# Optimization experiments

Measured on AMD Instinct MI355X. Metric: run time of the kernel, lower is better.

Reference implementation:

```python
import jax, jax.numpy as jnp
import numpy as np

DIM_H = 128
HEADS = 8
HEAD_DIM = DIM_H // HEADS
N_NODES = 40000
N_EDGES = 640000
BN_EPS = 1e-5


def setup_inputs() -> dict:
    key = jax.random.key(0)
    ks = jax.random.split(key, 16)
    s = 0.05
    x = jax.random.normal(ks[0], (N_NODES, DIM_H), dtype=jnp.float32)
    edge_index = jax.random.randint(ks[1], (2, N_EDGES), 0, N_NODES, dtype=jnp.int64)
    p = lambda k, shp: jax.random.normal(k, shp, dtype=jnp.float32) * s
    return {
        "x": x,
        "edge_index": edge_index,
        "Wk": p(ks[2], (DIM_H, DIM_H)), "bk": p(ks[3], (DIM_H,)),
        "Wv": p(ks[4], (DIM_H, DIM_H)), "bv": p(ks[5], (DIM_H,)),
        "Wo": p(ks[6], (DIM_H, DIM_H)), "bo": p(ks[7], (DIM_H,)),
        "bn1_g": jnp.ones((DIM_H,), jnp.float32), "bn1_b": jnp.zeros((DIM_H,), jnp.float32),
        "W1": p(ks[8], (2 * DIM_H, DIM_H)), "b1": p(ks[9], (2 * DIM_H,)),
        "W2": p(ks[10], (DIM_H, 2 * DIM_H)), "b2": p(ks[11], (DIM_H,)),
        "bn2_g": jnp.ones((DIM_H,), jnp.float32), "bn2_b": jnp.zeros((DIM_H,), jnp.float32),
    }


def _batchnorm(h, gamma, beta):
    # BatchNorm1d in training mode: per-feature batch mean / biased var over nodes
    mu = jnp.mean(h, axis=0)
    var = jnp.mean((h - mu) ** 2, axis=0)
    return (h - mu) * jax.lax.rsqrt(var + BN_EPS) * gamma + beta


def _sparse_attn(x, edge_index, Wk, bk, Wv, bv, Wo, bo):
    N = x.shape[0]
    src, dst = edge_index[0], edge_index[1]
    K = (x @ Wk.T + bk).reshape(N, HEADS, HEAD_DIM)
    V = (x @ Wv.T + bv).reshape(N, HEADS, HEAD_DIM)
    Q = x.reshape(N, HEADS, HEAD_DIM)  # query is raw h (no projection)
    # per-edge scores [E, H]
    scores = jnp.sum(K[src] * Q[dst], axis=-1) / np.sqrt(HEAD_DIM).astype(np.float32)
    # segment softmax over destination nodes (pyg_softmax)
    m = jax.ops.segment_max(scores, dst, num_segments=N)
    e = jnp.exp(scores - m[dst])
    denom = jax.ops.segment_sum(e, dst, num_segments=N)
    attn = e / (denom[dst] + 1e-16)  # [E, H]
    messages = V[src] * attn[:, :, None]  # [E, H, D]
    out = jax.ops.segment_sum(messages, dst, num_segments=N)  # [N, H, D]
    return out.reshape(N, DIM_H) @ Wo.T + bo


def reference(x, edge_index, Wk, bk, Wv, bv, Wo, bo, bn1_g, bn1_b,
              W1, b1, W2, b2, bn2_g, bn2_b):
    h_attn = _sparse_attn(x, edge_index, Wk, bk, Wv, bv, Wo, bo)
    h = _batchnorm(x + h_attn, bn1_g, bn1_b)
    ff = jax.nn.relu(h @ W1.T + b1) @ W2.T + b2
    h = _batchnorm(h + ff, bn2_g, bn2_b)
    return h
```

## Files before the change

### kernel.cpp

```cpp
#include <hip/hip_runtime.h>

#define DIM 128

typedef __attribute__((ext_vector_type(4))) _Float16 half4;
typedef __attribute__((ext_vector_type(8))) _Float16 half8;
typedef __attribute__((ext_vector_type(4))) float f32x4;

#define HP 136
#define UP 264

__global__ __launch_bounds__(256) void conv_wall(const float* __restrict__ Wk,
    const float* __restrict__ Wv, const float* __restrict__ Wo,
    const float* __restrict__ W1, const float* __restrict__ W2,
    _Float16* __restrict__ Wkh, _Float16* __restrict__ Wvh,
    _Float16* __restrict__ Woh, _Float16* __restrict__ W1h,
    _Float16* __restrict__ W2h, int* __restrict__ cnt, float* __restrict__ stats,
    int N) {
  int i = blockIdx.x * 256 + threadIdx.x;
  if (i < 16384) Wkh[i] = (_Float16)Wk[i];
  else if (i < 32768) Wvh[i - 16384] = (_Float16)Wv[i - 16384];
  else if (i < 49152) Woh[i - 32768] = (_Float16)Wo[i - 32768];
  else if (i < 81920) W1h[i - 49152] = (_Float16)W1[i - 49152];
  else W2h[i - 81920] = (_Float16)W2[i - 81920];
  if (i < N) cnt[i] = 0;
  if (i < 512) stats[i] = 0.f;
}

__global__ __launch_bounds__(256) void kv_mfma(const float* __restrict__ x,
    const _Float16* __restrict__ Wkh, const float* __restrict__ bk,
    const _Float16* __restrict__ Wvh, const float* __restrict__ bv,
    _Float16* __restrict__ KV, int N) {
  __shared__ _Float16 xs[64 * HP];
  int tid = threadIdx.x;
  int base = blockIdx.x * 64;
  int lane = tid & 63, w = tid >> 6;
  int l15 = lane & 15, quad = lane >> 4;

  for (int i = tid; i < 64 * 32; i += 256) {
    int m = i >> 5, c4 = i & 31;
    float4 tv = ((const float4*)x)[(size_t)(base + m) * 32 + c4];
    half4 hv;
    hv.x = (_Float16)tv.x; hv.y = (_Float16)tv.y;
    hv.z = (_Float16)tv.z; hv.w = (_Float16)tv.w;
    *(half4*)&xs[m * HP + c4 * 4] = hv;
  }
  __syncthreads();

  half8 afr[4][4];
#pragma unroll
  for (int mt = 0; mt < 4; mt++)
#pragma unroll
    for (int ks = 0; ks < 4; ks++)
      afr[mt][ks] = *(const half8*)&xs[(mt * 16 + l15) * HP + ks * 32 + quad * 8];

  const _Float16* W = (w < 2) ? Wkh : Wvh;
  const float* bias = (w < 2) ? bk : bv;
  int voff = (w < 2) ? 0 : 4;
  int c0 = (w & 1) * 64;

#pragma unroll
  for (int nt = 0; nt < 4; nt++) {
    int f = c0 + nt * 16 + l15;
    half8 bfr[4];
#pragma unroll
    for (int ks = 0; ks < 4; ks++)
      bfr[ks] = *(const half8*)&W[(size_t)f * 128 + ks * 32 + quad * 8];
    f32x4 acc[4];
#pragma unroll
    for (int mt = 0; mt < 4; mt++) acc[mt] = (f32x4){0.f, 0.f, 0.f, 0.f};
#pragma unroll
    for (int ks = 0; ks < 4; ks++)
#pragma unroll
      for (int mt = 0; mt < 4; mt++)
        acc[mt] = __builtin_amdgcn_mfma_f32_16x16x32_f16(afr[mt][ks], bfr[ks],
                                                          acc[mt], 0, 0, 0);
    float bb = bias[f];
    int fo = (f >> 2) * 8 + (f & 3) + voff;
#pragma unroll
    for (int mt = 0; mt < 4; mt++)
#pragma unroll
      for (int r = 0; r < 4; r++)
        KV[(size_t)(base + mt * 16 + quad * 4 + r) * 256 + fo] =
            (_Float16)(acc[mt][r] + bb);
  }
}

__global__ __launch_bounds__(256) void hist_rank(const int* __restrict__ ei,
    int* __restrict__ cnt, int* __restrict__ rank, int E) {
  int e = blockIdx.x * 256 + threadIdx.x;
  if (e < E) rank[e] = atomicAdd(&cnt[ei[E + e]], 1);
}

__global__ __launch_bounds__(256) void scanA(const int* __restrict__ cnt,
    int* __restrict__ rs, int* __restrict__ bsum, int N) {
  __shared__ int s[256];
  int t = threadIdx.x;
  int i = blockIdx.x * 256 + t;
  int v = (i < N) ? cnt[i] : 0;
  s[t] = v;
  __syncthreads();
  for (int off = 1; off < 256; off <<= 1) {
    int add = (t >= off) ? s[t - off] : 0;
    __syncthreads();
    s[t] += add;
    __syncthreads();
  }
  if (i < N) rs[i] = s[t] - v;
  if (t == 255) bsum[blockIdx.x] = s[t];
}

__global__ __launch_bounds__(256) void scanB(int* __restrict__ bsum, int nb) {
  __shared__ int s[256];
  int t = threadIdx.x;
  int v = (t < nb) ? bsum[t] : 0;
  s[t] = v;
  __syncthreads();
  for (int off = 1; off < 256; off <<= 1) {
    int add = (t >= off) ? s[t - off] : 0;
    __syncthreads();
    s[t] += add;
    __syncthreads();
  }
  if (t < nb) bsum[t] = s[t] - v;
}

__global__ __launch_bounds__(256) void scanC(int* __restrict__ rs,
    const int* __restrict__ bsum, int N, int E) {
  int i = blockIdx.x * 256 + threadIdx.x;
  if (i < N) rs[i] += bsum[blockIdx.x];
  if (i == 0) rs[N] = E;
}

__global__ __launch_bounds__(256) void scatter2(const int* __restrict__ ei,
    const int* __restrict__ rs, const int* __restrict__ rank,
    int* __restrict__ esrc, int E) {
  int e = blockIdx.x * 256 + threadIdx.x;
  if (e < E) esrc[rs[ei[E + e]] + rank[e]] = ei[e];
}

__global__ __launch_bounds__(256) void attn_agg(const _Float16* __restrict__ KV,
    const float* __restrict__ x, const int* __restrict__ rs,
    const int* __restrict__ esrc, _Float16* __restrict__ attn16, int N) {
  int wave = threadIdx.x >> 6, lane = threadIdx.x & 63;
  int n = blockIdx.x * 4 + wave;
  if (n >= N) return;
  int l = lane & 31, s = lane >> 5;
  float4 q = *(const float4*)&x[(size_t)n * DIM + 4 * l];
  int beg = rs[n], end = rs[n + 1];
  float a0 = 0.f, a1 = 0.f, a2 = 0.f, a3 = 0.f, dloc = 0.f;
  for (int e = beg + s; e < end; e += 8) {
    bool hh[4];
    int ss[4];
#pragma unroll
    for (int u = 0; u < 4; u++) hh[u] = (e + 2 * u) < end;
    ss[0] = esrc[e];
#pragma unroll
    for (int u = 1; u < 4; u++) ss[u] = hh[u] ? esrc[e + 2 * u] : ss[0];
    half8 kv[4];
#pragma unroll
    for (int u = 0; u < 4; u++)
      kv[u] = *(const half8*)&KV[(size_t)ss[u] * 256 + 8 * l];
    float p[4];
#pragma unroll
    for (int u = 0; u < 4; u++)
      p[u] = (float)kv[u][0] * q.x + (float)kv[u][1] * q.y +
             (float)kv[u][2] * q.z + (float)kv[u][3] * q.w;
#pragma unroll
    for (int u = 0; u < 4; u++) p[u] += __shfl_xor(p[u], 1);
#pragma unroll
    for (int u = 0; u < 4; u++) p[u] += __shfl_xor(p[u], 2);
    float ev[4];
#pragma unroll
    for (int u = 0; u < 4; u++) ev[u] = hh[u] ? __expf(p[u] * 0.25f) : 0.f;
#pragma unroll
    for (int u = 0; u < 4; u++) {
      dloc += ev[u];
      a0 += ev[u] * (float)kv[u][4];
      a1 += ev[u] * (float)kv[u][5];
      a2 += ev[u] * (float)kv[u][6];
      a3 += ev[u] * (float)kv[u][7];
    }
  }
  dloc += __shfl_xor(dloc, 32);
  a0 += __shfl_xor(a0, 32);
  a1 += __shfl_xor(a1, 32);
  a2 += __shfl_xor(a2, 32);
  a3 += __shfl_xor(a3, 32);
  if (s == 0) {
    float inv = 1.0f / (dloc + 1e-16f);
    half4 o;
    o.x = (_Float16)(a0 * inv);
    o.y = (_Float16)(a1 * inv);
    o.z = (_Float16)(a2 * inv);
    o.w = (_Float16)(a3 * inv);
    *(half4*)&attn16[(size_t)n * DIM + 4 * l] = o;
  }
}

__global__ __launch_bounds__(256) void o_proj_mfma(const _Float16* __restrict__ attn16,
    const float* __restrict__ x, const _Float16* __restrict__ Woh,
    const float* __restrict__ bo, float* __restrict__ t,
    float* __restrict__ stats, int N) {
  __shared__ _Float16 as16[64 * HP];
  int tid = threadIdx.x;
  int base = blockIdx.x * 64;
  int lane = tid & 63, w = tid >> 6;
  int l15 = lane & 15, quad = lane >> 4;

  for (int i = tid; i < 64 * 16; i += 256) {
    int m = i >> 4, c8 = i & 15;
    *(half8*)&as16[m * HP + c8 * 8] =
        ((const half8*)attn16)[(size_t)(base + m) * 16 + c8];
  }
  __syncthreads();

  half8 afr[4][4];
#pragma unroll
  for (int mt = 0; mt < 4; mt++)
#pragma unroll
    for (int ks = 0; ks < 4; ks++)
      afr[mt][ks] = *(const half8*)&as16[(mt * 16 + l15) * HP + ks * 32 + quad * 8];

  int c0 = w * 32;
  f32x4 acc[4][2];
#pragma unroll
  for (int mt = 0; mt < 4; mt++)
#pragma unroll
    for (int nt = 0; nt < 2; nt++) acc[mt][nt] = (f32x4){0.f, 0.f, 0.f, 0.f};
#pragma unroll
  for (int ks = 0; ks < 4; ks++) {
    half8 b[2];
#pragma unroll
    for (int nt = 0; nt < 2; nt++)
      b[nt] = *(const half8*)&Woh[(size_t)(c0 + nt * 16 + l15) * 128 + ks * 32 +
                                  quad * 8];
#pragma unroll
    for (int mt = 0; mt < 4; mt++)
#pragma unroll
      for (int nt = 0; nt < 2; nt++)
        acc[mt][nt] =
            __builtin_amdgcn_mfma_f32_16x16x32_f16(afr[mt][ks], b[nt], acc[mt][nt], 0, 0, 0);
  }

#pragma unroll
  for (int nt = 0; nt < 2; nt++) {
    int f = c0 + nt * 16 + l15;
    float bb = bo[f];
    float s = 0.f, q = 0.f;
#pragma unroll
    for (int mt = 0; mt < 4; mt++) {
#pragma unroll
      for (int r = 0; r < 4; r++) {
        int row = mt * 16 + quad * 4 + r;
        float tv = acc[mt][nt][r] + bb + x[(size_t)(base + row) * DIM + f];
        t[(size_t)(base + row) * DIM + f] = tv;
        s += tv;
        q += tv * tv;
      }
    }
    s += __shfl_xor(s, 16);
    s += __shfl_xor(s, 32);
    q += __shfl_xor(q, 16);
    q += __shfl_xor(q, 32);
    if (quad == 0) {
      atomicAdd(&stats[f], s);
      atomicAdd(&stats[128 + f], q);
    }
  }
}

__global__ __launch_bounds__(256) void ffn_mfma(const float* __restrict__ t,
    const float* __restrict__ stats1, const float* __restrict__ g1,
    const float* __restrict__ bb1, const _Float16* __restrict__ W1h,
    const float* __restrict__ b1, const _Float16* __restrict__ W2h,
    const float* __restrict__ b2, float* __restrict__ z,
    float* __restrict__ stats2, float invN, int N) {
  __shared__ _Float16 hs[64 * HP];
  __shared__ _Float16 us[64 * UP];
  __shared__ float cf[256];
  int tid = threadIdx.x;
  int base = blockIdx.x * 64;
  int lane = tid & 63, w = tid >> 6;
  int l15 = lane & 15, quad = lane >> 4;

  if (tid < 128) {
    float mu = stats1[tid] * invN;
    float var = stats1[128 + tid] * invN - mu * mu;
    float a = rsqrtf(var + 1e-5f) * g1[tid];
    cf[tid] = a;
    cf[128 + tid] = bb1[tid] - mu * a;
  }
  __syncthreads();

  for (int i = tid; i < 64 * 32; i += 256) {
    int m = i >> 5, c4 = i & 31;
    float4 tv = ((const float4*)t)[(size_t)(base + m) * 32 + c4];
    float4 ca = ((const float4*)cf)[c4];
    float4 cc = ((const float4*)cf)[32 + c4];
    half4 hv;
    hv.x = (_Float16)(tv.x * ca.x + cc.x);
    hv.y = (_Float16)(tv.y * ca.y + cc.y);
    hv.z = (_Float16)(tv.z * ca.z + cc.z);
    hv.w = (_Float16)(tv.w * ca.w + cc.w);
    *(half4*)&hs[m * HP + c4 * 4] = hv;
  }
  __syncthreads();

  int n0 = w * 64;
  half8 afr[4][4];
#pragma unroll
  for (int mt = 0; mt < 4; mt++)
#pragma unroll
    for (int ks = 0; ks < 4; ks++)
      afr[mt][ks] = *(const half8*)&hs[(mt * 16 + l15) * HP + ks * 32 + quad * 8];

#pragma unroll
  for (int nt = 0; nt < 4; nt++) {
    int n = n0 + nt * 16 + l15;
    half8 bfr[4];
#pragma unroll
    for (int ks = 0; ks < 4; ks++)
      bfr[ks] = *(const half8*)&W1h[(size_t)n * 128 + ks * 32 + quad * 8];
    f32x4 acc[4];
#pragma unroll
    for (int mt = 0; mt < 4; mt++) acc[mt] = (f32x4){0.f, 0.f, 0.f, 0.f};
#pragma unroll
    for (int ks = 0; ks < 4; ks++)
#pragma unroll
      for (int mt = 0; mt < 4; mt++)
        acc[mt] = __builtin_amdgcn_mfma_f32_16x16x32_f16(afr[mt][ks], bfr[ks],
                                                          acc[mt], 0, 0, 0);
    float bias = b1[n];
#pragma unroll
    for (int mt = 0; mt < 4; mt++)
#pragma unroll
      for (int r = 0; r < 4; r++)
        us[(mt * 16 + quad * 4 + r) * UP + n] =
            (_Float16)fmaxf(acc[mt][r] + bias, 0.f);
  }
  __syncthreads();

  int n2 = w * 32;
  f32x4 acc2[4][2];
#pragma unroll
  for (int mt = 0; mt < 4; mt++)
#pragma unroll
    for (int nt = 0; nt < 2; nt++) acc2[mt][nt] = (f32x4){0.f, 0.f, 0.f, 0.f};
  for (int ks = 0; ks < 8; ks++) {
    half8 a[4], b[2];
#pragma unroll
    for (int mt = 0; mt < 4; mt++)
      a[mt] = *(const half8*)&us[(mt * 16 + l15) * UP + ks * 32 + quad * 8];
#pragma unroll
    for (int nt = 0; nt < 2; nt++)
      b[nt] = *(const half8*)&W2h[(size_t)(n2 + nt * 16 + l15) * 256 + ks * 32 +
                                  quad * 8];
#pragma unroll
    for (int mt = 0; mt < 4; mt++)
#pragma unroll
      for (int nt = 0; nt < 2; nt++)
        acc2[mt][nt] =
            __builtin_amdgcn_mfma_f32_16x16x32_f16(a[mt], b[nt], acc2[mt][nt], 0, 0, 0);
  }

#pragma unroll
  for (int nt = 0; nt < 2; nt++) {
    int f = n2 + nt * 16 + l15;
    float bz = b2[f];
    float s = 0.f, q = 0.f;
#pragma unroll
    for (int mt = 0; mt < 4; mt++) {
#pragma unroll
      for (int r = 0; r < 4; r++) {
        int row = mt * 16 + quad * 4 + r;
        float hv = (float)hs[row * HP + f];
        float zv = hv + acc2[mt][nt][r] + bz;
        z[(size_t)(base + row) * DIM + f] = zv;
        s += zv;
        q += zv * zv;
      }
    }
    s += __shfl_xor(s, 16);
    s += __shfl_xor(s, 32);
    q += __shfl_xor(q, 16);
    q += __shfl_xor(q, 32);
    if (quad == 0) {
      atomicAdd(&stats2[f], s);
      atomicAdd(&stats2[128 + f], q);
    }
  }
}

__global__ __launch_bounds__(256) void final_apply(const float* __restrict__ z,
    const float* __restrict__ stats2, const float* __restrict__ g2,
    const float* __restrict__ bb2, float* __restrict__ out, float invN,
    int total4) {
  __shared__ float cf[256];
  int tid = threadIdx.x;
  if (tid < 128) {
    float mu = stats2[tid] * invN;
    float var = stats2[128 + tid] * invN - mu * mu;
    float a = rsqrtf(var + 1e-5f) * g2[tid];
    cf[tid] = a;
    cf[128 + tid] = bb2[tid] - mu * a;
  }
  __syncthreads();
  int i = blockIdx.x * 256 + tid;
  if (i >= total4) return;
  int f = (i * 4) & 127;
  float4 zv = ((const float4*)z)[i];
  float4 o;
  o.x = zv.x * cf[f] + cf[128 + f];
  o.y = zv.y * cf[f + 1] + cf[128 + f + 1];
  o.z = zv.z * cf[f + 2] + cf[128 + f + 2];
  o.w = zv.w * cf[f + 3] + cf[128 + f + 3];
  ((float4*)out)[i] = o;
}

extern "C" void kernel_launch(void* const* d_in, const int* in_sizes, int n_in,
                              void* d_out, int out_size, void* d_ws, size_t ws_size,
                              hipStream_t stream) {
  const float* x = (const float*)d_in[0];
  const int* ei = (const int*)d_in[1];
  const float* Wk = (const float*)d_in[2];
  const float* bk = (const float*)d_in[3];
  const float* Wv = (const float*)d_in[4];
  const float* bv = (const float*)d_in[5];
  const float* Wo = (const float*)d_in[6];
  const float* bo = (const float*)d_in[7];
  const float* bn1_g = (const float*)d_in[8];
  const float* bn1_b = (const float*)d_in[9];
  const float* W1 = (const float*)d_in[10];
  const float* b1 = (const float*)d_in[11];
  const float* W2 = (const float*)d_in[12];
  const float* b2 = (const float*)d_in[13];
  const float* bn2_g = (const float*)d_in[14];
  const float* bn2_b = (const float*)d_in[15];
  float* out = (float*)d_out;

  int N = in_sizes[0] / DIM;
  int E = in_sizes[1] / 2;

  _Float16* KV = (_Float16*)d_ws;
  _Float16* attn16 = KV + (size_t)N * 256;
  float* zbuf = (float*)(attn16 + (size_t)N * DIM);
  float* tbuf = (float*)d_ws;
  _Float16* W1h = (_Float16*)(zbuf + (size_t)N * DIM);
  _Float16* W2h = W1h + 32768;
  _Float16* Wkh = W2h + 32768;
  _Float16* Wvh = Wkh + 16384;
  _Float16* Woh = Wvh + 16384;
  float* stats = (float*)(Woh + 16384);
  int* cnt = (int*)(stats + 512);
  int* rs = cnt + N;
  int* rank = rs + N + 1;
  int* esrc = rank + E;
  int* bsum = esrc + E;

  int nblk = (N + 255) / 256;
  float invN = 1.0f / N;

  conv_wall<<<448, 256, 0, stream>>>(Wk, Wv, Wo, W1, W2, Wkh, Wvh, Woh, W1h, W2h,
                                     cnt, stats, N);
  kv_mfma<<<N / 64, 256, 0, stream>>>(x, Wkh, bk, Wvh, bv, KV, N);
  hist_rank<<<(E + 255) / 256, 256, 0, stream>>>(ei, cnt, rank, E);
  scanA<<<nblk, 256, 0, stream>>>(cnt, rs, bsum, N);
  scanB<<<1, 256, 0, stream>>>(bsum, nblk);
  scanC<<<nblk, 256, 0, stream>>>(rs, bsum, N, E);
  scatter2<<<(E + 255) / 256, 256, 0, stream>>>(ei, rs, rank, esrc, E);
  attn_agg<<<(N + 3) / 4, 256, 0, stream>>>(KV, x, rs, esrc, attn16, N);
  o_proj_mfma<<<N / 64, 256, 0, stream>>>(attn16, x, Woh, bo, tbuf, stats, N);
  ffn_mfma<<<N / 64, 256, 0, stream>>>(tbuf, stats, bn1_g, bn1_b, W1h, b1, W2h, b2,
                                       zbuf, stats + 256, invN, N);
  final_apply<<<((N * DIM / 4) + 255) / 256, 256, 0, stream>>>(
      zbuf, stats + 256, bn2_g, bn2_b, out, invN, N * DIM / 4);
}
```

Baseline: 260.4 us.

## Fuse CSR build into one cooperative kernel; use fp16 dot2 in attention

The five CSR-construction kernels (histogram/rank, three scan stages, scatter) are merged into a single cooperative kernel that uses grid-wide syncs between phases. The zeroing of counts and stats moves into it as well. This removes several launch gaps at the cost of grid.sync barriers and a fixed 640-block grid. Separately, attn_agg now computes the score dot products with fdot2 on fp16 pairs and accumulates the value-weighted sums in packed half2 rather than fp32. That cuts ALU work but lowers accumulation precision, so high-degree nodes risk larger error or overflow.

```diff
diff --git a/kernel.cpp b/kernel.cpp
--- a/kernel.cpp
+++ b/kernel.cpp
@@ -1,7 +1,11 @@
 #include <hip/hip_runtime.h>
+#include <hip/hip_cooperative_groups.h>
+
+namespace cg = cooperative_groups;
 
 #define DIM 128
 
+typedef __attribute__((ext_vector_type(2))) _Float16 half2_t;
 typedef __attribute__((ext_vector_type(4))) _Float16 half4;
 typedef __attribute__((ext_vector_type(8))) _Float16 half8;
 typedef __attribute__((ext_vector_type(4))) float f32x4;
@@ -14,16 +18,71 @@
     const float* __restrict__ W1, const float* __restrict__ W2,
     _Float16* __restrict__ Wkh, _Float16* __restrict__ Wvh,
     _Float16* __restrict__ Woh, _Float16* __restrict__ W1h,
-    _Float16* __restrict__ W2h, int* __restrict__ cnt, float* __restrict__ stats,
-    int N) {
+    _Float16* __restrict__ W2h) {
   int i = blockIdx.x * 256 + threadIdx.x;
   if (i < 16384) Wkh[i] = (_Float16)Wk[i];
   else if (i < 32768) Wvh[i - 16384] = (_Float16)Wv[i - 16384];
   else if (i < 49152) Woh[i - 32768] = (_Float16)Wo[i - 32768];
   else if (i < 81920) W1h[i - 49152] = (_Float16)W1[i - 49152];
   else W2h[i - 81920] = (_Float16)W2[i - 81920];
-  if (i < N) cnt[i] = 0;
-  if (i < 512) stats[i] = 0.f;
+}
+
+__global__ __launch_bounds__(256) void csr_coop(const int* __restrict__ ei,
+    int* __restrict__ cnt, int* __restrict__ rank, int* __restrict__ rs,
+    int* __restrict__ bsum, int* __restrict__ esrc, float* __restrict__ stats,
+    int N, int E) {
+  cg::grid_group grid = cg::this_grid();
+  __shared__ int sm[256];
+  int t = threadIdx.x;
+  int tid = blockIdx.x * 256 + t;
+  int nth = gridDim.x * 256;
+  int nchunk = (N + 255) / 256;
+
+  for (int i = tid; i < N; i += nth) cnt[i] = 0;
+  if (tid < 512) stats[tid] = 0.f;
+  grid.sync();
+
+  for (int e = tid; e < E; e += nth) rank[e] = atomicAdd(&cnt[ei[E + e]], 1);
+  grid.sync();
+
+  if (blockIdx.x < (unsigned)nchunk) {
+    int i = blockIdx.x * 256 + t;
+    int v = (i < N) ? cnt[i] : 0;
+    sm[t] = v;
+    __syncthreads();
+    for (int off = 1; off < 256; off <<= 1) {
+      int add = (t >= off) ? sm[t - off] : 0;
+      __syncthreads();
+      sm[t] += add;
+      __syncthreads();
+    }
+    if (i < N) rs[i] = sm[t] - v;
+    if (t == 255) bsum[blockIdx.x] = sm[t];
+  }
+  grid.sync();
+
+  if (blockIdx.x == 0) {
+    int v = (t < nchunk) ? bsum[t] : 0;
+    sm[t] = v;
+    __syncthreads();
+    for (int off = 1; off < 256; off <<= 1) {
+      int add = (t >= off) ? sm[t - off] : 0;
+      __syncthreads();
+      sm[t] += add;
+      __syncthreads();
+    }
+    if (t < nchunk) bsum[t] = sm[t] - v;
+  }
+  grid.sync();
+
+  if (blockIdx.x < (unsigned)nchunk) {
+    int i = blockIdx.x * 256 + t;
+    if (i < N) rs[i] += bsum[blockIdx.x];
+  }
+  if (tid == 0) rs[N] = E;
+  grid.sync();
+
+  for (int e = tid; e < E; e += nth) esrc[rs[ei[E + e]] + rank[e]] = ei[e];
 }
 
 __global__ __launch_bounds__(256) void kv_mfma(const float* __restrict__ x,
@@ -85,59 +144,6 @@
   }
 }
 
-__global__ __launch_bounds__(256) void hist_rank(const int* __restrict__ ei,
-    int* __restrict__ cnt, int* __restrict__ rank, int E) {
-  int e = blockIdx.x * 256 + threadIdx.x;
-  if (e < E) rank[e] = atomicAdd(&cnt[ei[E + e]], 1);
-}
-
-__global__ __launch_bounds__(256) void scanA(const int* __restrict__ cnt,
-    int* __restrict__ rs, int* __restrict__ bsum, int N) {
-  __shared__ int s[256];
-  int t = threadIdx.x;
-  int i = blockIdx.x * 256 + t;
-  int v = (i < N) ? cnt[i] : 0;
-  s[t] = v;
-  __syncthreads();
-  for (int off = 1; off < 256; off <<= 1) {
-    int add = (t >= off) ? s[t - off] : 0;
-    __syncthreads();
-    s[t] += add;
-    __syncthreads();
-  }
-  if (i < N) rs[i] = s[t] - v;
-  if (t == 255) bsum[blockIdx.x] = s[t];
-}
-
-__global__ __launch_bounds__(256) void scanB(int* __restrict__ bsum, int nb) {
-  __shared__ int s[256];
-  int t = threadIdx.x;
-  int v = (t < nb) ? bsum[t] : 0;
-  s[t] = v;
-  __syncthreads();
-  for (int off = 1; off < 256; off <<= 1) {
-    int add = (t >= off) ? s[t - off] : 0;
-    __syncthreads();
-    s[t] += add;
-    __syncthreads();
-  }
-  if (t < nb) bsum[t] = s[t] - v;
-}
-
-__global__ __launch_bounds__(256) void scanC(int* __restrict__ rs,
-    const int* __restrict__ bsum, int N, int E) {
-  int i = blockIdx.x * 256 + threadIdx.x;
-  if (i < N) rs[i] += bsum[blockIdx.x];
-  if (i == 0) rs[N] = E;
-}
-
-__global__ __launch_bounds__(256) void scatter2(const int* __restrict__ ei,
-    const int* __restrict__ rs, const int* __restrict__ rank,
-    int* __restrict__ esrc, int E) {
-  int e = blockIdx.x * 256 + threadIdx.x;
-  if (e < E) esrc[rs[ei[E + e]] + rank[e]] = ei[e];
-}
-
 __global__ __launch_bounds__(256) void attn_agg(const _Float16* __restrict__ KV,
     const float* __restrict__ x, const int* __restrict__ rs,
     const int* __restrict__ esrc, _Float16* __restrict__ attn16, int N) {
@@ -146,8 +152,12 @@
   if (n >= N) return;
   int l = lane & 31, s = lane >> 5;
   float4 q = *(const float4*)&x[(size_t)n * DIM + 4 * l];
+  half2_t q01 = {(_Float16)q.x, (_Float16)q.y};
+  half2_t q23 = {(_Float16)q.z, (_Float16)q.w};
   int beg = rs[n], end = rs[n + 1];
-  float a0 = 0.f, a1 = 0.f, a2 = 0.f, a3 = 0.f, dloc = 0.f;
+  half2_t a01 = {(_Float16)0.f, (_Float16)0.f};
+  half2_t a23 = a01;
+  float dloc = 0.f;
   for (int e = beg + s; e < end; e += 8) {
     bool hh[4];
     int ss[4];
@@ -162,25 +172,30 @@
       kv[u] = *(const half8*)&KV[(size_t)ss[u] * 256 + 8 * l];
     float p[4];
 #pragma unroll
-    for (int u = 0; u < 4; u++)
-      p[u] = (float)kv[u][0] * q.x + (float)kv[u][1] * q.y +
-             (float)kv[u][2] * q.z + (float)kv[u][3] * q.w;
+    for (int u = 0; u < 4; u++) {
+      half2_t k01 = {kv[u][0], kv[u][1]};
+      half2_t k23 = {kv[u][2], kv[u][3]};
+      p[u] = __builtin_amdgcn_fdot2(k01, q01,
+              __builtin_amdgcn_fdot2(k23, q23, 0.f, false), false);
+    }
 #pragma unroll
     for (int u = 0; u < 4; u++) p[u] += __shfl_xor(p[u], 1);
 #pragma unroll
     for (int u = 0; u < 4; u++) p[u] += __shfl_xor(p[u], 2);
-    float ev[4];
-#pragma unroll
-    for (int u = 0; u < 4; u++) ev[u] = hh[u] ? __expf(p[u] * 0.25f) : 0.f;
 #pragma unroll
     for (int u = 0; u < 4; u++) {
-      dloc += ev[u];
-      a0 += ev[u] * (float)kv[u][4];
-      a1 += ev[u] * (float)kv[u][5];
-      a2 += ev[u] * (float)kv[u][6];
-      a3 += ev[u] * (float)kv[u][7];
-    }
-  }
+      float ev = hh[u] ? __expf(p[u] * 0.25f) : 0.f;
+      dloc += ev;
+      _Float16 eh = (_Float16)ev;
+      half2_t e2 = {eh, eh};
+      half2_t v01 = {kv[u][4], kv[u][5]};
+      half2_t v23 = {kv[u][6], kv[u][7]};
+      a01 += e2 * v01;
+      a23 += e2 * v23;
+    }
+  }
+  float a0 = (float)a01[0], a1 = (float)a01[1];
+  float a2 = (float)a23[0], a3 = (float)a23[1];
   dloc += __shfl_xor(dloc, 32);
   a0 += __shfl_xor(a0, 32);
   a1 += __shfl_xor(a1, 32);
@@ -457,17 +472,17 @@
   int* esrc = rank + E;
   int* bsum = esrc + E;
 
-  int nblk = (N + 255) / 256;
   float invN = 1.0f / N;
 
-  conv_wall<<<448, 256, 0, stream>>>(Wk, Wv, Wo, W1, W2, Wkh, Wvh, Woh, W1h, W2h,
-                                     cnt, stats, N);
+  conv_wall<<<448, 256, 0, stream>>>(Wk, Wv, Wo, W1, W2, Wkh, Wvh, Woh, W1h, W2h);
   kv_mfma<<<N / 64, 256, 0, stream>>>(x, Wkh, bk, Wvh, bv, KV, N);
-  hist_rank<<<(E + 255) / 256, 256, 0, stream>>>(ei, cnt, rank, E);
-  scanA<<<nblk, 256, 0, stream>>>(cnt, rs, bsum, N);
-  scanB<<<1, 256, 0, stream>>>(bsum, nblk);
-  scanC<<<nblk, 256, 0, stream>>>(rs, bsum, N, E);
-  scatter2<<<(E + 255) / 256, 256, 0, stream>>>(ei, rs, rank, esrc, E);
+  {
+    void* args[] = {(void*)&ei, (void*)&cnt, (void*)&rank, (void*)&rs,
+                    (void*)&bsum, (void*)&esrc, (void*)&stats, (void*)&N,
+                    (void*)&E};
+    hipLaunchCooperativeKernel(reinterpret_cast<void*>(csr_coop), dim3(640),
+                               dim3(256), args, 0, stream);
+  }
   attn_agg<<<(N + 3) / 4, 256, 0, stream>>>(KV, x, rs, esrc, attn16, N);
   o_proj_mfma<<<N / 64, 256, 0, stream>>>(attn16, x, Woh, bo, tbuf, stats, N);
   ffn_mfma<<<N / 64, 256, 0, stream>>>(tbuf, stats, bn1_g, bn1_b, W1h, b1, W2h, b2,
```

Result: slower. 612.5 us (+135.2%).

## Store K/V in FP8 and shard destination-degree histogram counters

Applied to the files above, without the earlier changes.

The K/V projection output is now stored as FP8 (E4M3) bytes instead of fp16, halving the per-edge gather traffic in the attention aggregation kernel, which unpacks the values with hardware fp8-to-f32 conversions. Separately, the histogram atomics are spread over 8 shard copies keyed by edge index to reduce contention, with the scan summing the shards and emitting per-shard offsets for the scatter. The FP8 storage adds quantization error to keys and values and may break accuracy tolerance. It also moves tbuf to its own region rather than aliasing the KV buffer.

```diff
diff --git a/kernel.cpp b/kernel.cpp
--- a/kernel.cpp
+++ b/kernel.cpp
@@ -1,13 +1,19 @@
 #include <hip/hip_runtime.h>
 
 #define DIM 128
-
+#define NSHARD 8
+
+typedef __attribute__((ext_vector_type(2))) float f32x2;
 typedef __attribute__((ext_vector_type(4))) _Float16 half4;
 typedef __attribute__((ext_vector_type(8))) _Float16 half8;
 typedef __attribute__((ext_vector_type(4))) float f32x4;
 
 #define HP 136
 #define UP 264
+
+__device__ __forceinline__ unsigned char to_fp8(float v) {
+  return (unsigned char)(__builtin_amdgcn_cvt_pk_fp8_f32(v, v, 0, false) & 0xff);
+}
 
 __global__ __launch_bounds__(256) void conv_wall(const float* __restrict__ Wk,
     const float* __restrict__ Wv, const float* __restrict__ Wo,
@@ -17,19 +23,20 @@
     _Float16* __restrict__ W2h, int* __restrict__ cnt, float* __restrict__ stats,
     int N) {
   int i = blockIdx.x * 256 + threadIdx.x;
+  int nth = gridDim.x * 256;
   if (i < 16384) Wkh[i] = (_Float16)Wk[i];
   else if (i < 32768) Wvh[i - 16384] = (_Float16)Wv[i - 16384];
   else if (i < 49152) Woh[i - 32768] = (_Float16)Wo[i - 32768];
   else if (i < 81920) W1h[i - 49152] = (_Float16)W1[i - 49152];
-  else W2h[i - 81920] = (_Float16)W2[i - 81920];
-  if (i < N) cnt[i] = 0;
+  else if (i < 114688) W2h[i - 81920] = (_Float16)W2[i - 81920];
+  for (int j = i; j < N * NSHARD; j += nth) cnt[j] = 0;
   if (i < 512) stats[i] = 0.f;
 }
 
 __global__ __launch_bounds__(256) void kv_mfma(const float* __restrict__ x,
     const _Float16* __restrict__ Wkh, const float* __restrict__ bk,
     const _Float16* __restrict__ Wvh, const float* __restrict__ bv,
-    _Float16* __restrict__ KV, int N) {
+    unsigned char* __restrict__ KV8, int N) {
   __shared__ _Float16 xs[64 * HP];
   int tid = threadIdx.x;
   int base = blockIdx.x * 64;
@@ -80,15 +87,15 @@
     for (int mt = 0; mt < 4; mt++)
 #pragma unroll
       for (int r = 0; r < 4; r++)
-        KV[(size_t)(base + mt * 16 + quad * 4 + r) * 256 + fo] =
-            (_Float16)(acc[mt][r] + bb);
+        KV8[(size_t)(base + mt * 16 + quad * 4 + r) * 256 + fo] =
+            to_fp8(acc[mt][r] + bb);
   }
 }
 
 __global__ __launch_bounds__(256) void hist_rank(const int* __restrict__ ei,
-    int* __restrict__ cnt, int* __restrict__ rank, int E) {
+    int* __restrict__ cnt, int* __restrict__ rank, int N, int E) {
   int e = blockIdx.x * 256 + threadIdx.x;
-  if (e < E) rank[e] = atomicAdd(&cnt[ei[E + e]], 1);
+  if (e < E) rank[e] = atomicAdd(&cnt[(e & (NSHARD - 1)) * N + ei[E + e]], 1);
 }
 
 __global__ __launch_bounds__(256) void scanA(const int* __restrict__ cnt,
@@ -96,7 +103,10 @@
   __shared__ int s[256];
   int t = threadIdx.x;
   int i = blockIdx.x * 256 + t;
-  int v = (i < N) ? cnt[i] : 0;
+  int v = 0;
+  if (i < N)
+#pragma unroll
+    for (int sh = 0; sh < NSHARD; sh++) v += cnt[sh * N + i];
   s[t] = v;
   __syncthreads();
   for (int off = 1; off < 256; off <<= 1) {
@@ -125,20 +135,30 @@
 }
 
 __global__ __launch_bounds__(256) void scanC(int* __restrict__ rs,
-    const int* __restrict__ bsum, int N, int E) {
+    const int* __restrict__ bsum, const int* __restrict__ cnt,
+    int* __restrict__ rs_shard, int N, int E) {
   int i = blockIdx.x * 256 + threadIdx.x;
-  if (i < N) rs[i] += bsum[blockIdx.x];
+  if (i < N) {
+    int b = rs[i] + bsum[blockIdx.x];
+    rs[i] = b;
+#pragma unroll
+    for (int sh = 0; sh < NSHARD; sh++) {
+      rs_shard[sh * N + i] = b;
+      b += cnt[sh * N + i];
+    }
+  }
   if (i == 0) rs[N] = E;
 }
 
 __global__ __launch_bounds__(256) void scatter2(const int* __restrict__ ei,
-    const int* __restrict__ rs, const int* __restrict__ rank,
-    int* __restrict__ esrc, int E) {
+    const int* __restrict__ rs_shard, const int* __restrict__ rank,
+    int* __restrict__ esrc, int N, int E) {
   int e = blockIdx.x * 256 + threadIdx.x;
-  if (e < E) esrc[rs[ei[E + e]] + rank[e]] = ei[e];
-}
-
-__global__ __launch_bounds__(256) void attn_agg(const _Float16* __restrict__ KV,
+  if (e < E)
+    esrc[rs_shard[(e & (NSHARD - 1)) * N + ei[E + e]] + rank[e]] = ei[e];
+}
+
+__global__ __launch_bounds__(256) void attn_agg(const unsigned char* __restrict__ KV8,
     const float* __restrict__ x, const int* __restrict__ rs,
     const int* __restrict__ esrc, _Float16* __restrict__ attn16, int N) {
   int wave = threadIdx.x >> 6, lane = threadIdx.x & 63;
@@ -156,29 +176,31 @@
     ss[0] = esrc[e];
 #pragma unroll
     for (int u = 1; u < 4; u++) ss[u] = hh[u] ? esrc[e + 2 * u] : ss[0];
-    half8 kv[4];
+    uint2 kv[4];
 #pragma unroll
     for (int u = 0; u < 4; u++)
-      kv[u] = *(const half8*)&KV[(size_t)ss[u] * 256 + 8 * l];
+      kv[u] = *(const uint2*)&KV8[(size_t)ss[u] * 256 + 8 * l];
     float p[4];
 #pragma unroll
-    for (int u = 0; u < 4; u++)
-      p[u] = (float)kv[u][0] * q.x + (float)kv[u][1] * q.y +
-             (float)kv[u][2] * q.z + (float)kv[u][3] * q.w;
+    for (int u = 0; u < 4; u++) {
+      f32x2 k01 = __builtin_amdgcn_cvt_pk_f32_fp8(kv[u].x, false);
+      f32x2 k23 = __builtin_amdgcn_cvt_pk_f32_fp8(kv[u].x, true);
+      p[u] = k01[0] * q.x + k01[1] * q.y + k23[0] * q.z + k23[1] * q.w;
+    }
 #pragma unroll
     for (int u = 0; u < 4; u++) p[u] += __shfl_xor(p[u], 1);
 #pragma unroll
     for (int u = 0; u < 4; u++) p[u] += __shfl_xor(p[u], 2);
-    float ev[4];
-#pragma unroll
-    for (int u = 0; u < 4; u++) ev[u] = hh[u] ? __expf(p[u] * 0.25f) : 0.f;
 #pragma unroll
     for (int u = 0; u < 4; u++) {
-      dloc += ev[u];
-      a0 += ev[u] * (float)kv[u][4];
-      a1 += ev[u] * (float)kv[u][5];
-      a2 += ev[u] * (float)kv[u][6];
-      a3 += ev[u] * (float)kv[u][7];
+      float ev = hh[u] ? __expf(p[u] * 0.25f) : 0.f;
+      dloc += ev;
+      f32x2 v01 = __builtin_amdgcn_cvt_pk_f32_fp8(kv[u].y, false);
+      f32x2 v23 = __builtin_amdgcn_cvt_pk_f32_fp8(kv[u].y, true);
+      a0 += ev * v01[0];
+      a1 += ev * v01[1];
+      a2 += ev * v23[0];
+      a3 += ev * v23[1];
     }
   }
   dloc += __shfl_xor(dloc, 32);
@@ -441,34 +463,35 @@
   int N = in_sizes[0] / DIM;
   int E = in_sizes[1] / 2;
 
-  _Float16* KV = (_Float16*)d_ws;
-  _Float16* attn16 = KV + (size_t)N * 256;
+  unsigned char* KV8 = (unsigned char*)d_ws;
+  _Float16* attn16 = (_Float16*)(KV8 + (size_t)N * 256);
   float* zbuf = (float*)(attn16 + (size_t)N * DIM);
-  float* tbuf = (float*)d_ws;
-  _Float16* W1h = (_Float16*)(zbuf + (size_t)N * DIM);
+  float* tbuf = zbuf + (size_t)N * DIM;
+  _Float16* W1h = (_Float16*)(tbuf + (size_t)N * DIM);
   _Float16* W2h = W1h + 32768;
   _Float16* Wkh = W2h + 32768;
   _Float16* Wvh = Wkh + 16384;
   _Float16* Woh = Wvh + 16384;
   float* stats = (float*)(Woh + 16384);
   int* cnt = (int*)(stats + 512);
-  int* rs = cnt + N;
-  int* rank = rs + N + 1;
+  int* rs = cnt + (size_t)N * NSHARD;
+  int* rs_shard = rs + N + 1;
+  int* rank = rs_shard + (size_t)N * NSHARD;
   int* esrc = rank + E;
   int* bsum = esrc + E;
 
   int nblk = (N + 255) / 256;
   float invN = 1.0f / N;
 
-  conv_wall<<<448, 256, 0, stream>>>(Wk, Wv, Wo, W1, W2, Wkh, Wvh, Woh, W1h, W2h,
+  conv_wall<<<512, 256, 0, stream>>>(Wk, Wv, Wo, W1, W2, Wkh, Wvh, Woh, W1h, W2h,
                                      cnt, stats, N);
-  kv_mfma<<<N / 64, 256, 0, stream>>>(x, Wkh, bk, Wvh, bv, KV, N);
-  hist_rank<<<(E + 255) / 256, 256, 0, stream>>>(ei, cnt, rank, E);
+  kv_mfma<<<N / 64, 256, 0, stream>>>(x, Wkh, bk, Wvh, bv, KV8, N);
+  hist_rank<<<(E + 255) / 256, 256, 0, stream>>>(ei, cnt, rank, N, E);
   scanA<<<nblk, 256, 0, stream>>>(cnt, rs, bsum, N);
   scanB<<<1, 256, 0, stream>>>(bsum, nblk);
-  scanC<<<nblk, 256, 0, stream>>>(rs, bsum, N, E);
-  scatter2<<<(E + 255) / 256, 256, 0, stream>>>(ei, rs, rank, esrc, E);
-  attn_agg<<<(N + 3) / 4, 256, 0, stream>>>(KV, x, rs, esrc, attn16, N);
+  scanC<<<nblk, 256, 0, stream>>>(rs, bsum, cnt, rs_shard, N, E);
+  scatter2<<<(E + 255) / 256, 256, 0, stream>>>(ei, rs_shard, rank, esrc, N, E);
+  attn_agg<<<(N + 3) / 4, 256, 0, stream>>>(KV8, x, rs, esrc, attn16, N);
   o_proj_mfma<<<N / 64, 256, 0, stream>>>(attn16, x, Woh, bo, tbuf, stats, N);
   ffn_mfma<<<N / 64, 256, 0, stream>>>(tbuf, stats, bn1_g, bn1_b, W1h, b1, W2h, b2,
                                        zbuf, stats + 256, invN, N);
```

Result: faster. 251.3 us (-3.5%).
